# Kernel optimization log

Measured on AMD Instinct MI355X. Metric: run time of the kernel, lower is better.

## Reference

```python
import jax, jax.numpy as jnp
import numpy as np

EPS = 1e-5
HEADS = 24
HEAD_DIM = 128


def _layernorm_noaffine(x):
    # LayerNorm over last dim (head_dim), elementwise_affine=False
    mu = jnp.mean(x, axis=-1, keepdims=True)
    var = jnp.mean(jnp.square(x - mu), axis=-1, keepdims=True)
    return (x - mu) / jnp.sqrt(var + EPS)


def _apply_rope(x, cos, sin):
    # diffusers apply_rotary_emb, use_real_unbind_dim=-2, sequence_dim=1
    # x: [B, S_img, H, D]; cos/sin: [S_img, D]
    x_real, x_imag = jnp.split(x, 2, axis=-1)               # halves of D
    x_rot = jnp.concatenate([-x_imag, x_real], axis=-1)
    return x * cos[None, :, None, :] + x_rot * sin[None, :, None, :]


def setup_inputs() -> dict:
    key = jax.random.key(0)
    ks = jax.random.split(key, 8)
    B, T, I, D = 2, 256, 1024, 3072
    inner = HEADS * HEAD_DIM
    return {
        "hidden_states": jax.random.normal(ks[0], (B, I, D), jnp.float32),
        "encoder_hidden_states": jax.random.normal(ks[1], (B, T, D), jnp.float32),
        "cos": jax.random.uniform(ks[2], (I, HEAD_DIM), jnp.float32),
        "sin": jax.random.uniform(ks[3], (I, HEAD_DIM), jnp.float32),
        "w_qkv": jax.random.normal(ks[4], (D, 3 * inner), jnp.float32) * 0.02,
        "b_qkv": jax.random.normal(ks[5], (3 * inner,), jnp.float32) * 0.02,
        "w_out": jax.random.normal(ks[6], (inner, D), jnp.float32) * 0.02,
        "b_out": jax.random.normal(ks[7], (D,), jnp.float32) * 0.02,
    }


def reference(hidden_states, encoder_hidden_states, cos, sin, w_qkv, b_qkv, w_out, b_out):
    text_len = encoder_hidden_states.shape[1]
    x = jnp.concatenate([encoder_hidden_states, hidden_states], axis=1)  # [B, S, D]
    B, S, _ = x.shape
    qkv = x @ w_qkv + b_qkv                                  # [B, S, 3*inner]
    q, k, v = jnp.split(qkv, 3, axis=-1)
    q = q.reshape(B, S, HEADS, HEAD_DIM)
    k = k.reshape(B, S, HEADS, HEAD_DIM)
    v = v.reshape(B, S, HEADS, HEAD_DIM)
    q = _layernorm_noaffine(q)
    k = _layernorm_noaffine(k)
    # partial RoPE: image tokens only
    q = jnp.concatenate([q[:, :text_len], _apply_rope(q[:, text_len:], cos, sin)], axis=1)
    k = jnp.concatenate([k[:, :text_len], _apply_rope(k[:, text_len:], cos, sin)], axis=1)
    # non-causal attention, scale = 1/sqrt(head_dim)
    scale = 1.0 / np.sqrt(HEAD_DIM).astype(np.float32)
    scores = jnp.einsum('bqhd,bkhd->bhqk', q, k) * scale
    attn = jax.nn.softmax(scores, axis=-1)
    out = jnp.einsum('bhqk,bkhd->bqhd', attn, v).reshape(B, S, HEADS * HEAD_DIM)
    out = out @ w_out + b_out                                # [B, S, D]
    return out[:, text_len:, :], out[:, :text_len, :]
```

## Files before the change

### kernel.cpp

```cpp
#include <hip/hip_runtime.h>

typedef unsigned short u16;
typedef __attribute__((ext_vector_type(8))) short bf16x8;
typedef __attribute__((ext_vector_type(4))) float f32x4;
typedef __attribute__((ext_vector_type(16))) float f32x16;

typedef const __attribute__((address_space(1))) void* gptr_t;
typedef __attribute__((address_space(3))) void* lptr_t;

__device__ __forceinline__ unsigned cvtpk_bf16(float a, float b){
  unsigned r; asm("v_cvt_pk_bf16_f32 %0, %1, %2" : "=v"(r) : "v"(a), "v"(b)); return r;
}
__device__ __forceinline__ u16 f2bf(float x){ return (u16)cvtpk_bf16(x, x); }
__device__ __forceinline__ float bf2f(u16 u){ union{unsigned i; float f;} v; v.i = ((unsigned)u)<<16; return v.f; }
__device__ __forceinline__ float fexp2(float x){ float r; asm("v_exp_f32 %0, %1" : "=v"(r) : "v"(x)); return r; }

__global__ __launch_bounds__(256) void prep_x_kernel(const float* __restrict__ hs,
                                                     const float* __restrict__ ehs,
                                                     u16* __restrict__ A){
  int idx = blockIdx.x*256 + threadIdx.x;
  int v = idx*4;
  int m = v/3072, c = v - m*3072;
  int b = m/1280, s = m - b*1280;
  const float* src = (s < 256) ? (ehs + ((size_t)(b*256+s))*3072 + c)
                               : (hs  + ((size_t)(b*1024+(s-256)))*3072 + c);
  float4 f = *(const float4*)src;
  uint2 o; o.x = cvtpk_bf16(f.x, f.y); o.y = cvtpk_bf16(f.z, f.w);
  *(uint2*)(A + v) = o;
}

__global__ __launch_bounds__(256) void transpose_w_kernel(const float* __restrict__ W,
                                                          u16* __restrict__ Wt,
                                                          int K, int N){
  __shared__ float t[64][36];
  int k0 = blockIdx.y*64, n0 = blockIdx.x*32;
  int tid = threadIdx.x;
  #pragma unroll
  for (int i=0;i<2;i++){
    int cell = i*256 + tid; int kl = cell>>3, nc = cell&7;
    *(float4*)&t[kl][nc*4] = *(const float4*)&W[(size_t)(k0+kl)*N + n0 + nc*4];
  }
  __syncthreads();
  #pragma unroll
  for (int i=0;i<2;i++){
    int chunk = i*256 + tid; int nl = chunk>>4, kc = chunk&15;
    float a = t[kc*4+0][nl], b2 = t[kc*4+1][nl], c2 = t[kc*4+2][nl], d2 = t[kc*4+3][nl];
    uint2 u; u.x = cvtpk_bf16(a, b2); u.y = cvtpk_bf16(c2, d2);
    *(uint2*)&Wt[(size_t)(n0+nl)*K + k0 + kc*4] = u;
  }
}

template<int EPI>
__global__ __launch_bounds__(256) void gemm_bt_kernel(const u16* __restrict__ A,
                                                      const u16* __restrict__ Bt,
                                                      const float* __restrict__ bias,
                                                      u16* __restrict__ Cb, float* __restrict__ Cf,
                                                      int K, int N){
  __shared__ u16 As[2][4096];
  __shared__ u16 Bs[2][4096];
  int tid = threadIdx.x, wv = tid>>6, lane = tid&63;
  int l15 = lane & 15, l4 = lane >> 4;
  int m0 = blockIdx.y*128, n0 = blockIdx.x*128;
  int wr = wv>>1, wc = wv&1;

  f32x4 acc[4][4];
  #pragma unroll
  for (int i=0;i<4;i++)
    #pragma unroll
    for (int j=0;j<4;j++)
      #pragma unroll
      for (int r=0;r<4;r++) acc[i][j][r] = 0.f;

  const int NT = K >> 5;

  auto stage = [&](int buf, int kt){
    #pragma unroll
    for (int i=0;i<2;i++){
      int c = (wv*2+i)*64 + lane; int row = c>>2, kc = c&3;
      const u16* s = A + (size_t)(m0+row)*K + kt + kc*8;
      __builtin_amdgcn_global_load_lds((gptr_t)s, (lptr_t)(&As[buf][(wv*2+i)*512]), 16, 0, 0);
    }
    #pragma unroll
    for (int i=0;i<2;i++){
      int c = (wv*2+i)*64 + lane; int row = c>>2, kc = c&3;
      const u16* s = Bt + (size_t)(n0+row)*K + kt + kc*8;
      __builtin_amdgcn_global_load_lds((gptr_t)s, (lptr_t)(&Bs[buf][(wv*2+i)*512]), 16, 0, 0);
    }
  };

  stage(0, 0);
  __syncthreads();
  for (int t=0; t<NT; t++){
    int cur = t & 1;
    if (t+1 < NT) stage(cur^1, (t+1)*32);
    bf16x8 af[4], bfr[4];
    #pragma unroll
    for (int i=0;i<4;i++){
      af[i]  = *(const bf16x8*)&As[cur][(wr*64 + i*16 + l15)*32 + l4*8];
      bfr[i] = *(const bf16x8*)&Bs[cur][(wc*64 + i*16 + l15)*32 + l4*8];
    }
    #pragma unroll
    for (int i=0;i<4;i++)
      #pragma unroll
      for (int j=0;j<4;j++)
        acc[i][j] = __builtin_amdgcn_mfma_f32_16x16x32_bf16(af[i], bfr[j], acc[i][j], 0,0,0);
    __syncthreads();
  }

  #pragma unroll
  for (int i=0;i<4;i++){
    int row = m0 + wr*64 + i*16 + l4*4;
    #pragma unroll
    for (int j=0;j<4;j++){
      int col = n0 + wc*64 + j*16 + l15;
      float bv = bias[col];
      if (EPI == 0){
        #pragma unroll
        for (int r=0;r<4;r++)
          Cb[(size_t)(row+r)*N + col] = f2bf(acc[i][j][r] + bv);
      } else {
        #pragma unroll
        for (int r=0;r<4;r++){
          int rr = row + r;
          int bb = rr / 1280; int s = rr - bb*1280;
          float* dst = (s < 256) ? (Cf + 6291456 + ((size_t)(bb*256 + s))*3072)
                                 : (Cf + ((size_t)(bb*1024 + (s-256)))*3072);
          dst[col] = acc[i][j][r] + bv;
        }
      }
    }
  }
}

__device__ __forceinline__ void ln_head(const u16* __restrict__ in, u16* __restrict__ out,
                                        const float* __restrict__ cosb, const float* __restrict__ sinb,
                                        int lane, int s, float scale){
  float x0 = bf2f(in[lane]), x1 = bf2f(in[64+lane]);
  float sum = x0 + x1;
  #pragma unroll
  for (int off=32; off>=1; off>>=1) sum += __shfl_xor(sum, off);
  float mean = sum * 0.0078125f;
  float d0 = x0-mean, d1 = x1-mean;
  float vs = d0*d0 + d1*d1;
  #pragma unroll
  for (int off=32; off>=1; off>>=1) vs += __shfl_xor(vs, off);
  float rstd = rsqrtf(vs*0.0078125f + 1e-5f);
  float y0 = d0*rstd, y1 = d1*rstd;
  if (s >= 256){
    int p = s - 256;
    float c0 = cosb[p*128 + lane], c1 = cosb[p*128 + 64 + lane];
    float s0 = sinb[p*128 + lane], s1 = sinb[p*128 + 64 + lane];
    float t0 = y0*c0 - y1*s0;
    float t1 = y1*c1 + y0*s1;
    y0 = t0; y1 = t1;
  }
  out[lane]    = f2bf(y0*scale);
  out[64+lane] = f2bf(y1*scale);
}

__global__ __launch_bounds__(256) void ln_rope_kernel(const u16* __restrict__ qkv,
                                                      const float* __restrict__ cosb,
                                                      const float* __restrict__ sinb,
                                                      u16* __restrict__ Q, u16* __restrict__ Kd){
  int g = blockIdx.x*4 + (threadIdx.x>>6);
  int lane = threadIdx.x & 63;
  int h = g % 24; int m = g / 24;
  int b = m / 1280; int s = m - b*1280;
  const u16* base = qkv + (size_t)m*9216 + h*128;
  size_t ho = ((size_t)(b*24 + h)*1280 + s)*128;
  ln_head(base,        Q  + ho, cosb, sinb, lane, s, 0.12751512f);
  ln_head(base + 3072, Kd + ho, cosb, sinb, lane, s, 1.0f);
}

__global__ __launch_bounds__(256) void v_transpose_kernel(const u16* __restrict__ qkv,
                                                          u16* __restrict__ Vt){
  __shared__ u16 tl[16384];
  int tid = threadIdx.x;
  int blk = blockIdx.x;
  int st = blk % 10; int bh = blk / 10; int b = bh/24, h = bh - b*24;
  #pragma unroll
  for (int i=0;i<8;i++){
    int idx = i*256 + tid; int s = idx>>4, dc = idx&15;
    int m = b*1280 + st*128 + s;
    bf16x8 v = *(const bf16x8*)(qkv + (size_t)m*9216 + 6144 + h*128 + dc*8);
    *(bf16x8*)(tl + (s*16 + (dc ^ ((s>>3)&7)))*8) = v;
  }
  __syncthreads();
  #pragma unroll
  for (int i=0;i<8;i++){
    int idx = i*256 + tid; int d = idx>>4, sc = idx&15;
    union { u16 t[8]; bf16x8 v; } tmp;
    #pragma unroll
    for (int j=0;j<8;j++){
      int s = sc*8 + j;
      tmp.t[j] = tl[(s*16 + ((d>>3) ^ ((s>>3)&7)))*8 + (d&7)];
    }
    *(bf16x8*)(Vt + ((size_t)bh*128 + d)*1280 + st*128 + sc*8) = tmp.v;
  }
}

__global__ __launch_bounds__(256) void attn_kernel(const u16* __restrict__ Q,
                                                   const u16* __restrict__ Kg,
                                                   const u16* __restrict__ Vt,
                                                   u16* __restrict__ AO){
  __shared__ u16 smem[16384];
  u16* Ks = smem;
  u16* Vs = smem + 8192;
  int tid = threadIdx.x, wv = tid>>6, lane = tid&63;
  int l31 = lane & 31, hi = lane >> 5;
  int blk = blockIdx.x;
  int qt = blk % 10; int bh = blk / 10;
  int b = bh / 24; int h = bh - b*24;
  const u16* Qb = Q  + (size_t)bh*1280*128;
  const u16* Kb = Kg + (size_t)bh*1280*128;
  const u16* Vb = Vt + (size_t)bh*128*1280;
  int q0 = qt*128 + wv*32;

  bf16x8 qf[8];
  #pragma unroll
  for (int ds=0; ds<8; ds++)
    qf[ds] = *(const bf16x8*)(Qb + (size_t)(q0 + l31)*128 + ds*16 + hi*8);

  f32x16 o[4];
  #pragma unroll
  for (int dc=0; dc<4; dc++)
    #pragma unroll
    for (int r=0;r<16;r++) o[dc][r] = 0.f;
  float mrun = -1e30f, lrun = 0.f;

  for (int t=0; t<20; t++){
    int s0 = t*64;
    __syncthreads();
    #pragma unroll
    for (int i=0;i<4;i++){
      int c = (wv*4+i)*64 + lane; int key = c>>4, dc16 = c&15;
      const u16* src = Kb + (size_t)(s0+key)*128 + ((dc16 ^ (key&7))<<3);
      __builtin_amdgcn_global_load_lds((gptr_t)src, (lptr_t)(Ks + (wv*4+i)*512), 16, 0, 0);
    }
    #pragma unroll
    for (int i=0;i<4;i++){
      int c = (wv*4+i)*64 + lane; int d = c>>3, kc = c&7;
      const u16* src = Vb + (size_t)d*1280 + s0 + ((kc ^ (d&7))<<3);
      __builtin_amdgcn_global_load_lds((gptr_t)src, (lptr_t)(Vs + (wv*4+i)*512), 16, 0, 0);
    }
    __syncthreads();

    f32x16 sacc0, sacc1;
    #pragma unroll
    for (int r=0;r<16;r++){ sacc0[r]=0.f; sacc1[r]=0.f; }
    #pragma unroll
    for (int ds=0; ds<8; ds++){
      int ch = ds*2 + hi;
      bf16x8 k0 = *(const bf16x8*)(Ks + (l31*16      + (ch ^ (l31 & 7)))*8);
      bf16x8 k1 = *(const bf16x8*)(Ks + ((32+l31)*16 + (ch ^ (l31 & 7)))*8);
      sacc0 = __builtin_amdgcn_mfma_f32_32x32x16_bf16(k0, qf[ds], sacc0, 0,0,0);
      sacc1 = __builtin_amdgcn_mfma_f32_32x32x16_bf16(k1, qf[ds], sacc1, 0,0,0);
    }
    float mt = sacc0[0];
    #pragma unroll
    for (int r=1;r<16;r++) mt = fmaxf(mt, sacc0[r]);
    #pragma unroll
    for (int r=0;r<16;r++) mt = fmaxf(mt, sacc1[r]);
    mt = fmaxf(mt, __shfl_xor(mt, 32));
    float mnew = fmaxf(mrun, mt);
    float corr = fexp2(mrun - mnew);
    mrun = mnew;
    float p[32]; float ps = 0.f;
    #pragma unroll
    for (int r=0;r<16;r++){ p[r]    = fexp2(sacc0[r] - mnew); ps += p[r]; }
    #pragma unroll
    for (int r=0;r<16;r++){ p[16+r] = fexp2(sacc1[r] - mnew); ps += p[16+r]; }
    ps += __shfl_xor(ps, 32);
    lrun = lrun*corr + ps;
    #pragma unroll
    for (int dc=0; dc<4; dc++)
      #pragma unroll
      for (int r=0;r<16;r++) o[dc][r] *= corr;

    bf16x8 pf[4];
    #pragma unroll
    for (int c=0;c<4;c++){
      const float* pp = p + (c>>1)*16 + (c&1)*8;
      unsigned x0 = cvtpk_bf16(pp[0], pp[1]);
      unsigned y0 = cvtpk_bf16(pp[4], pp[5]);
      unsigned x1 = cvtpk_bf16(pp[2], pp[3]);
      unsigned y1 = cvtpk_bf16(pp[6], pp[7]);
      asm volatile("v_permlane32_swap_b32 %0, %1" : "+v"(x0), "+v"(y0));
      asm volatile("v_permlane32_swap_b32 %0, %1" : "+v"(x1), "+v"(y1));
      union { unsigned u[4]; bf16x8 v; } wb;
      wb.u[0]=x0; wb.u[1]=x1; wb.u[2]=y0; wb.u[3]=y1;
      pf[c] = wb.v;
    }
    #pragma unroll
    for (int c=0;c<4;c++){
      #pragma unroll
      for (int dc=0;dc<4;dc++){
        int d = dc*32 + l31;
        bf16x8 vf = *(const bf16x8*)(Vs + (d*8 + ((2*c+hi) ^ (d&7)))*8);
        o[dc] = __builtin_amdgcn_mfma_f32_32x32x16_bf16(vf, pf[c], o[dc], 0,0,0);
      }
    }
  }

  float rl = 1.f / lrun;
  __syncthreads();
  u16* ob = smem + wv*4096;
  #pragma unroll
  for (int dc=0; dc<4; dc++){
    #pragma unroll
    for (int rp=0; rp<8; rp++){
      int d = dc*32 + 2*(rp&1) + 8*(rp>>1) + 4*hi;
      unsigned u = cvtpk_bf16(o[dc][2*rp]*rl, o[dc][2*rp+1]*rl);
      int chs = (d>>3) ^ (l31 & 7);
      *(unsigned*)(ob + l31*128 + chs*8 + (d&7)) = u;
    }
  }
  __syncthreads();
  #pragma unroll
  for (int i=0;i<8;i++){
    int idx = i*64 + lane; int q = idx>>4, c8 = idx&15;
    bf16x8 vv = *(const bf16x8*)(ob + q*128 + ((c8 ^ (q&7))<<3));
    *(bf16x8*)(AO + (size_t)(b*1280 + q0 + q)*3072 + h*128 + c8*8) = vv;
  }
}

extern "C" void kernel_launch(void* const* d_in, const int* in_sizes, int n_in,
                              void* d_out, int out_size, void* d_ws, size_t ws_size,
                              hipStream_t stream){
  (void)in_sizes; (void)n_in; (void)out_size; (void)ws_size;
  const float* hs   = (const float*)d_in[0];
  const float* ehs  = (const float*)d_in[1];
  const float* cosb = (const float*)d_in[2];
  const float* sinb = (const float*)d_in[3];
  const float* wqkv = (const float*)d_in[4];
  const float* bqkv = (const float*)d_in[5];
  const float* wout = (const float*)d_in[6];
  const float* bout = (const float*)d_in[7];
  char* w = (char*)d_ws;
  size_t o = 0;
  u16* Abf = (u16*)(w + o); o += 15728640ull;
  u16* WqT = (u16*)(w + o); o += 56623104ull;
  u16* WoT = (u16*)(w + o); o += 18874368ull;
  u16* qkv = (u16*)(w + o); o += 47185920ull;
  u16* Qd  = (u16*)(w + o); o += 15728640ull;
  u16* Kd  = (u16*)(w + o); o += 15728640ull;
  u16* Vtd = (u16*)(w + o); o += 15728640ull;
  u16* AO  = (u16*)(w + o);
  float* out = (float*)d_out;

  prep_x_kernel<<<7680, 256, 0, stream>>>(hs, ehs, Abf);
  transpose_w_kernel<<<dim3(288,48), 256, 0, stream>>>(wqkv, WqT, 3072, 9216);
  transpose_w_kernel<<<dim3(96,48),  256, 0, stream>>>(wout, WoT, 3072, 3072);
  gemm_bt_kernel<0><<<dim3(72,20), 256, 0, stream>>>(Abf, WqT, bqkv, qkv, nullptr, 3072, 9216);
  ln_rope_kernel<<<15360, 256, 0, stream>>>(qkv, cosb, sinb, Qd, Kd);
  v_transpose_kernel<<<480, 256, 0, stream>>>(qkv, Vtd);
  attn_kernel<<<480, 256, 0, stream>>>(Qd, Kd, Vtd, AO);
  gemm_bt_kernel<1><<<dim3(24,20), 256, 0, stream>>>(AO, WoT, bout, nullptr, out, 3072, 3072);
}
```

Baseline: 586.1 us.

## Add 256x256 pipelined QKV GEMM and double-buffer K/V loads in attention

New measurement: 572.0 us. -2.4%, faster.

```diff
diff --git a/kernel.cpp b/kernel.cpp
--- a/kernel.cpp
+++ b/kernel.cpp
@@ -50,11 +50,101 @@
   }
 }
 
-template<int EPI>
+__global__ __launch_bounds__(512) void gemm256_kernel(const u16* __restrict__ A,
+                                                      const u16* __restrict__ Bt,
+                                                      const float* __restrict__ bias,
+                                                      u16* __restrict__ C){
+  const int K = 3072, N = 9216;
+  __shared__ __align__(16) u16 lds[2][2][2][8192];
+  int tid = threadIdx.x, wv = tid>>6, lane = tid&63;
+  int wm = wv>>2, wn = wv&3;
+  int l15 = lane&15, l4 = lane>>4;
+
+  int bid = blockIdx.x;
+  int wg = (bid&7)*45 + (bid>>3);
+  int bm = wg/36, bn = wg%36;
+  int m0 = bm*256, n0 = bn*256;
+
+  int srow = tid>>2;
+  int schn = (tid&3) ^ ((tid>>3)&3);
+  const u16* aSrc = A  + (size_t)(m0 + srow)*K + schn*8;
+  const u16* bSrc = Bt + (size_t)(n0 + srow)*K + schn*8;
+  u16* ldsF = &lds[0][0][0][0];
+
+  auto stagePair = [&](int Gp){
+    int s = (Gp>>1)&1, h = Gp&1;
+    size_t ko = (size_t)Gp*32;
+    u16* la = ldsF + s*32768 + h*8192 + wv*512;
+    u16* lb = la + 16384;
+    const u16* a0 = aSrc + ko;
+    const u16* b0 = bSrc + ko;
+    __builtin_amdgcn_global_load_lds((gptr_t)a0,                 (lptr_t)la,        16,0,0);
+    __builtin_amdgcn_global_load_lds((gptr_t)(a0+(size_t)128*K), (lptr_t)(la+4096), 16,0,0);
+    __builtin_amdgcn_global_load_lds((gptr_t)b0,                 (lptr_t)lb,        16,0,0);
+    __builtin_amdgcn_global_load_lds((gptr_t)(b0+(size_t)128*K), (lptr_t)(lb+4096), 16,0,0);
+  };
+
+  int fcs = l4 ^ ((l15>>1)&3);
+  int aoff = (wm*128 + l15)*32 + fcs*8;
+  int boff = (wn*64  + l15)*32 + fcs*8;
+
+  f32x4 acc[8][4];
+  #pragma unroll
+  for (int r=0;r<8;r++)
+    #pragma unroll
+    for (int c=0;c<4;c++)
+      #pragma unroll
+      for (int q=0;q<4;q++) acc[r][c][q] = 0.f;
+
+  stagePair(0); stagePair(1); stagePair(2);
+  asm volatile("s_waitcnt vmcnt(8)" ::: "memory");
+  __builtin_amdgcn_s_barrier();
+
+  auto group = [&](int G, bool issue){
+    const u16* rA = ldsF + ((G>>1)&1)*32768 + (G&1)*8192;
+    const u16* rB = rA + 16384;
+    bf16x8 af[8], bfv[4];
+    #pragma unroll
+    for (int r=0;r<8;r++) af[r] = *(const bf16x8*)(rA + aoff + r*512);
+    #pragma unroll
+    for (int c=0;c<4;c++) bfv[c] = *(const bf16x8*)(rB + boff + c*512);
+    if (issue) stagePair(G+3);
+    __builtin_amdgcn_s_setprio(1);
+    #pragma unroll
+    for (int r=0;r<8;r++)
+      #pragma unroll
+      for (int c=0;c<4;c++)
+        acc[r][c] = __builtin_amdgcn_mfma_f32_16x16x32_bf16(af[r], bfv[c], acc[r][c], 0,0,0);
+    __builtin_amdgcn_s_setprio(0);
+  };
+
+  for (int G=0; G<93; ++G){
+    group(G, true);
+    asm volatile("s_waitcnt vmcnt(8)" ::: "memory");
+    __builtin_amdgcn_s_barrier();
+  }
+  group(93,false); asm volatile("s_waitcnt vmcnt(4)" ::: "memory"); __builtin_amdgcn_s_barrier();
+  group(94,false); asm volatile("s_waitcnt vmcnt(0)" ::: "memory"); __builtin_amdgcn_s_barrier();
+  group(95,false);
+
+  #pragma unroll
+  for (int r=0;r<8;r++){
+    int row = m0 + wm*128 + r*16 + l4*4;
+    #pragma unroll
+    for (int c=0;c<4;c++){
+      int col = n0 + wn*64 + c*16 + l15;
+      float bv = bias[col];
+      #pragma unroll
+      for (int q=0;q<4;q++)
+        C[(size_t)(row+q)*N + col] = f2bf(acc[r][c][q] + bv);
+    }
+  }
+}
+
 __global__ __launch_bounds__(256) void gemm_bt_kernel(const u16* __restrict__ A,
                                                       const u16* __restrict__ Bt,
                                                       const float* __restrict__ bias,
-                                                      u16* __restrict__ Cb, float* __restrict__ Cf,
+                                                      float* __restrict__ Cf,
                                                       int K, int N){
   __shared__ u16 As[2][4096];
   __shared__ u16 Bs[2][4096];
@@ -114,19 +204,13 @@
     for (int j=0;j<4;j++){
       int col = n0 + wc*64 + j*16 + l15;
       float bv = bias[col];
-      if (EPI == 0){
-        #pragma unroll
-        for (int r=0;r<4;r++)
-          Cb[(size_t)(row+r)*N + col] = f2bf(acc[i][j][r] + bv);
-      } else {
-        #pragma unroll
-        for (int r=0;r<4;r++){
-          int rr = row + r;
-          int bb = rr / 1280; int s = rr - bb*1280;
-          float* dst = (s < 256) ? (Cf + 6291456 + ((size_t)(bb*256 + s))*3072)
-                                 : (Cf + ((size_t)(bb*1024 + (s-256)))*3072);
-          dst[col] = acc[i][j][r] + bv;
-        }
+      #pragma unroll
+      for (int r=0;r<4;r++){
+        int rr = row + r;
+        int bb = rr / 1280; int s = rr - bb*1280;
+        float* dst = (s < 256) ? (Cf + 6291456 + ((size_t)(bb*256 + s))*3072)
+                               : (Cf + ((size_t)(bb*1024 + (s-256)))*3072);
+        dst[col] = acc[i][j][r] + bv;
       }
     }
   }
@@ -203,9 +287,7 @@
                                                    const u16* __restrict__ Kg,
                                                    const u16* __restrict__ Vt,
                                                    u16* __restrict__ AO){
-  __shared__ u16 smem[16384];
-  u16* Ks = smem;
-  u16* Vs = smem + 8192;
+  __shared__ __align__(16) u16 smem[32768];
   int tid = threadIdx.x, wv = tid>>6, lane = tid&63;
   int l31 = lane & 31, hi = lane >> 5;
   int blk = blockIdx.x;
@@ -228,26 +310,31 @@
     for (int r=0;r<16;r++) o[dc][r] = 0.f;
   float mrun = -1e30f, lrun = 0.f;
 
-  for (int t=0; t<20; t++){
-    int s0 = t*64;
-    __syncthreads();
+  auto stage = [&](int t){
+    int s0 = t*64; int bu = t&1;
+    u16* Ksb = smem + bu*8192;
+    u16* Vsb = smem + 16384 + bu*8192;
     #pragma unroll
     for (int i=0;i<4;i++){
       int c = (wv*4+i)*64 + lane; int key = c>>4, dc16 = c&15;
       const u16* src = Kb + (size_t)(s0+key)*128 + ((dc16 ^ (key&7))<<3);
-      __builtin_amdgcn_global_load_lds((gptr_t)src, (lptr_t)(Ks + (wv*4+i)*512), 16, 0, 0);
+      __builtin_amdgcn_global_load_lds((gptr_t)src, (lptr_t)(Ksb + (wv*4+i)*512), 16, 0, 0);
     }
     #pragma unroll
     for (int i=0;i<4;i++){
       int c = (wv*4+i)*64 + lane; int d = c>>3, kc = c&7;
       const u16* src = Vb + (size_t)d*1280 + s0 + ((kc ^ (d&7))<<3);
-      __builtin_amdgcn_global_load_lds((gptr_t)src, (lptr_t)(Vs + (wv*4+i)*512), 16, 0, 0);
-    }
-    __syncthreads();
-
+      __builtin_amdgcn_global_load_lds((gptr_t)src, (lptr_t)(Vsb + (wv*4+i)*512), 16, 0, 0);
+    }
+  };
+
+  auto compute = [&](int t){
+    const u16* Ks = smem + (t&1)*8192;
+    const u16* Vs = smem + 16384 + (t&1)*8192;
     f32x16 sacc0, sacc1;
     #pragma unroll
     for (int r=0;r<16;r++){ sacc0[r]=0.f; sacc1[r]=0.f; }
+    __builtin_amdgcn_s_setprio(1);
     #pragma unroll
     for (int ds=0; ds<8; ds++){
       int ch = ds*2 + hi;
@@ -256,6 +343,7 @@
       sacc0 = __builtin_amdgcn_mfma_f32_32x32x16_bf16(k0, qf[ds], sacc0, 0,0,0);
       sacc1 = __builtin_amdgcn_mfma_f32_32x32x16_bf16(k1, qf[ds], sacc1, 0,0,0);
     }
+    __builtin_amdgcn_s_setprio(0);
     float mt = sacc0[0];
     #pragma unroll
     for (int r=1;r<16;r++) mt = fmaxf(mt, sacc0[r]);
@@ -291,6 +379,7 @@
       wb.u[0]=x0; wb.u[1]=x1; wb.u[2]=y0; wb.u[3]=y1;
       pf[c] = wb.v;
     }
+    __builtin_amdgcn_s_setprio(1);
     #pragma unroll
     for (int c=0;c<4;c++){
       #pragma unroll
@@ -300,7 +389,20 @@
         o[dc] = __builtin_amdgcn_mfma_f32_32x32x16_bf16(vf, pf[c], o[dc], 0,0,0);
       }
     }
-  }
+    __builtin_amdgcn_s_setprio(0);
+  };
+
+  stage(0); stage(1);
+  for (int t=0; t<19; ++t){
+    asm volatile("s_waitcnt vmcnt(8)" ::: "memory");
+    __builtin_amdgcn_s_barrier();
+    compute(t);
+    __builtin_amdgcn_s_barrier();
+    if (t <= 17) stage(t+2);
+  }
+  asm volatile("s_waitcnt vmcnt(0)" ::: "memory");
+  __builtin_amdgcn_s_barrier();
+  compute(19);
 
   float rl = 1.f / lrun;
   __syncthreads();
@@ -351,9 +453,9 @@
   prep_x_kernel<<<7680, 256, 0, stream>>>(hs, ehs, Abf);
   transpose_w_kernel<<<dim3(288,48), 256, 0, stream>>>(wqkv, WqT, 3072, 9216);
   transpose_w_kernel<<<dim3(96,48),  256, 0, stream>>>(wout, WoT, 3072, 3072);
-  gemm_bt_kernel<0><<<dim3(72,20), 256, 0, stream>>>(Abf, WqT, bqkv, qkv, nullptr, 3072, 9216);
+  gemm256_kernel<<<360, 512, 0, stream>>>(Abf, WqT, bqkv, qkv);
   ln_rope_kernel<<<15360, 256, 0, stream>>>(qkv, cosb, sinb, Qd, Kd);
   v_transpose_kernel<<<480, 256, 0, stream>>>(qkv, Vtd);
   attn_kernel<<<480, 256, 0, stream>>>(Qd, Kd, Vtd, AO);
-  gemm_bt_kernel<1><<<dim3(24,20), 256, 0, stream>>>(AO, WoT, bout, nullptr, out, 3072, 3072);
-}
+  gemm_bt_kernel<<<dim3(24,20), 256, 0, stream>>>(AO, WoT, bout, out, 3072, 3072);
+}
```
